# Optimization experiments

Measured on AMD Instinct MI355X. Metric: run time of the kernel, lower is better.

Reference implementation:

```python
import jax, jax.numpy as jnp
import numpy as np

# Module config (matches init_kwargs)
ANCHORS = np.array([[4.0, 4.0, 4.0], [8.0, 8.0, 8.0], [16.0, 16.0, 16.0]], dtype=np.float32)  # (w,h,d) per anchor
NUM_CLASSES = 1
IMG_SIZE = (96, 96, 96)  # (W, H, D)

B, A = 16, 3
ATTRS = 5 + NUM_CLASSES
D = H = W = 48


def setup_inputs() -> dict:
    key = jax.random.key(0)
    inp = jax.random.normal(key, (B, A * ATTRS, D, H, W), dtype=jnp.float32)
    return {"inp": inp}


def reference(inp):
    b, _, d, h, w = inp.shape
    stride_w = IMG_SIZE[0] / w
    stride_h = IMG_SIZE[1] / h
    stride_d = IMG_SIZE[2] / d

    # [B, A, D, H, W, attrs]
    pred = inp.reshape(b, A, ATTRS, d, h, w).transpose(0, 1, 3, 4, 5, 2)

    x = jax.nn.sigmoid(pred[..., 0])
    y = jax.nn.sigmoid(pred[..., 1])
    z = jax.nn.sigmoid(pred[..., 2])
    l = pred[..., 3]
    conf = jax.nn.sigmoid(pred[..., 4])
    pred_cls = jax.nn.sigmoid(pred[..., 5:])

    # Broadcast grids (replaces the nested python-loop fills)
    grid_x = jnp.arange(w, dtype=inp.dtype)                    # (W,) -> last axis
    grid_y = jnp.arange(h, dtype=inp.dtype)[:, None]           # (H,1)
    grid_z = jnp.arange(d, dtype=inp.dtype)[:, None, None]     # (D,1,1)

    # Original uses scaled anchor WIDTH for the length channel
    anchor_len = (jnp.asarray(ANCHORS[:, 0], dtype=inp.dtype) / stride_w)[None, :, None, None, None]

    bx = (x + grid_x) * stride_w
    by = (y + grid_y) * stride_h
    bz = (z + grid_z) * stride_d
    bl = jnp.exp(l) * anchor_len * stride_w

    boxes = jnp.stack([bx, by, bz, bl], axis=-1)  # [B,A,D,H,W,4]

    out = jnp.concatenate(
        [boxes.reshape(b, -1, 4), conf.reshape(b, -1, 1), pred_cls.reshape(b, -1, NUM_CLASSES)],
        axis=-1,
    )
    return out
```

## Files before the change

### kernel.cpp

```cpp
#include <hip/hip_runtime.h>


#define DHW   110592
#define HW48  2304
#define PAIRS 55296
#define NTOT  2654208

__device__ __forceinline__ float sigm(float v) {
    return 1.0f / (1.0f + __expf(-v));
}

__global__ __launch_bounds__(256) void DecodeBox_kernel(
    const float* __restrict__ in, float* __restrict__ out) {
    int t = blockIdx.x * blockDim.x + threadIdx.x;
    if (t >= NTOT) return;

    int s2 = t % PAIRS;
    int ba = t / PAIRS;
    int a  = ba % 3;
    int b  = ba / 3;

    int s  = 2 * s2;
    int x0 = s % 48;
    int y0 = (s / 48) % 48;
    int z0 = s / HW48;

    const float anchw = (a == 0) ? 4.0f : (a == 1) ? 8.0f : 16.0f;

    const float* ip = in + (size_t)(b * 18 + a * 6) * DHW + s;
    float2 tx = *(const float2*)(ip + 0 * DHW);
    float2 ty = *(const float2*)(ip + 1 * DHW);
    float2 tz = *(const float2*)(ip + 2 * DHW);
    float2 tl = *(const float2*)(ip + 3 * DHW);
    float2 tc = *(const float2*)(ip + 4 * DHW);
    float2 tk = *(const float2*)(ip + 5 * DHW);

    float bx0 = (sigm(tx.x) + (float)x0) * 2.0f;
    float by0 = (sigm(ty.x) + (float)y0) * 2.0f;
    float bz0 = (sigm(tz.x) + (float)z0) * 2.0f;
    float bl0 = __expf(tl.x) * anchw;
    float cf0 = sigm(tc.x);
    float cl0 = sigm(tk.x);
    float bx1 = (sigm(tx.y) + (float)(x0 + 1)) * 2.0f;
    float by1 = (sigm(ty.y) + (float)y0) * 2.0f;
    float bz1 = (sigm(tz.y) + (float)z0) * 2.0f;
    float bl1 = __expf(tl.y) * anchw;
    float cf1 = sigm(tc.y);
    float cl1 = sigm(tk.y);

    float4* op = (float4*)(out + (size_t)ba * (DHW * 6) + (size_t)12 * s2);
    op[0] = make_float4(bx0, by0, bz0, bl0);
    op[1] = make_float4(cf0, cl0, bx1, by1);
    op[2] = make_float4(bz1, bl1, cf1, cl1);
}

extern "C" void kernel_launch(void* const* d_in, const int* in_sizes, int n_in,
                              void* d_out, int out_size, void* d_ws, size_t ws_size,
                              hipStream_t stream) {
    const float* in = (const float*)d_in[0];
    float* out = (float*)d_out;
    const int threads = 256;
    const int blocks = (NTOT + threads - 1) / threads;
    DecodeBox_kernel<<<blocks, threads, 0, stream>>>(in, out);
}
```

Before: 223.1 us.

## Stage interleaved outputs through swizzled LDS for coalesced float4 stores

Each thread now processes four consecutive spatial positions with float4 loads instead of two with float2 loads. Outputs are written to shared memory with an XOR swizzle to avoid bank conflicts, then written back so consecutive lanes store consecutive float4s. This is meant to remove the strided 48-byte-per-lane store pattern that wastes write bandwidth. The cost is an LDS round-trip and a block barrier per tile.

```diff
diff --git a/kernel.cpp b/kernel.cpp
--- a/kernel.cpp
+++ b/kernel.cpp
@@ -3,55 +3,78 @@
 
 #define DHW   110592
 #define HW48  2304
-#define PAIRS 55296
-#define NTOT  2654208
+#define SPB   1024
+#define BPP   108
+#define F4B   1536
+#define F4P   165888
+#define NBLK  5184
 
 __device__ __forceinline__ float sigm(float v) {
     return 1.0f / (1.0f + __expf(-v));
 }
 
+__device__ __forceinline__ int swz(int i) {
+    return (i & ~7) | ((i ^ (i >> 3)) & 7);
+}
+
 __global__ __launch_bounds__(256) void DecodeBox_kernel(
     const float* __restrict__ in, float* __restrict__ out) {
-    int t = blockIdx.x * blockDim.x + threadIdx.x;
-    if (t >= NTOT) return;
+    __shared__ float4 lds[F4B];
 
-    int s2 = t % PAIRS;
-    int ba = t / PAIRS;
-    int a  = ba % 3;
-    int b  = ba / 3;
+    const int tid   = threadIdx.x;
+    const int blk   = blockIdx.x;
+    const int p     = blk / BPP;
+    const int chunk = blk - p * BPP;
+    const int a     = p % 3;
 
-    int s  = 2 * s2;
-    int x0 = s % 48;
-    int y0 = (s / 48) % 48;
-    int z0 = s / HW48;
-
+    const int S  = chunk * SPB + tid * 4;
+    const int x0 = S % 48;
+    const float yf = (float)((S / 48) % 48);
+    const float zf = (float)(S / HW48);
     const float anchw = (a == 0) ? 4.0f : (a == 1) ? 8.0f : 16.0f;
 
-    const float* ip = in + (size_t)(b * 18 + a * 6) * DHW + s;
-    float2 tx = *(const float2*)(ip + 0 * DHW);
-    float2 ty = *(const float2*)(ip + 1 * DHW);
-    float2 tz = *(const float2*)(ip + 2 * DHW);
-    float2 tl = *(const float2*)(ip + 3 * DHW);
-    float2 tc = *(const float2*)(ip + 4 * DHW);
-    float2 tk = *(const float2*)(ip + 5 * DHW);
+    const float* ip = in + (size_t)p * (6 * DHW) + S;
+    float4 tx = *(const float4*)(ip + 0 * DHW);
+    float4 ty = *(const float4*)(ip + 1 * DHW);
+    float4 tz = *(const float4*)(ip + 2 * DHW);
+    float4 tl = *(const float4*)(ip + 3 * DHW);
+    float4 tc = *(const float4*)(ip + 4 * DHW);
+    float4 tk = *(const float4*)(ip + 5 * DHW);
 
-    float bx0 = (sigm(tx.x) + (float)x0) * 2.0f;
-    float by0 = (sigm(ty.x) + (float)y0) * 2.0f;
-    float bz0 = (sigm(tz.x) + (float)z0) * 2.0f;
-    float bl0 = __expf(tl.x) * anchw;
-    float cf0 = sigm(tc.x);
-    float cl0 = sigm(tk.x);
-    float bx1 = (sigm(tx.y) + (float)(x0 + 1)) * 2.0f;
-    float by1 = (sigm(ty.y) + (float)y0) * 2.0f;
-    float bz1 = (sigm(tz.y) + (float)z0) * 2.0f;
-    float bl1 = __expf(tl.y) * anchw;
-    float cf1 = sigm(tc.y);
-    float cl1 = sigm(tk.y);
+    const float* txp = (const float*)&tx;
+    const float* typ = (const float*)&ty;
+    const float* tzp = (const float*)&tz;
+    const float* tlp = (const float*)&tl;
+    const float* tcp = (const float*)&tc;
+    const float* tkp = (const float*)&tk;
 
-    float4* op = (float4*)(out + (size_t)ba * (DHW * 6) + (size_t)12 * s2);
-    op[0] = make_float4(bx0, by0, bz0, bl0);
-    op[1] = make_float4(cf0, cl0, bx1, by1);
-    op[2] = make_float4(bz1, bl1, cf1, cl1);
+    float bx[4], by[4], bz[4], bl[4], cf[4], cl[4];
+#pragma unroll
+    for (int q = 0; q < 4; ++q) {
+        bx[q] = (sigm(txp[q]) + (float)(x0 + q)) * 2.0f;
+        by[q] = (sigm(typ[q]) + yf) * 2.0f;
+        bz[q] = (sigm(tzp[q]) + zf) * 2.0f;
+        bl[q] = __expf(tlp[q]) * anchw;
+        cf[q] = sigm(tcp[q]);
+        cl[q] = sigm(tkp[q]);
+    }
+
+    const int wb = 6 * tid;
+    lds[swz(wb + 0)] = make_float4(bx[0], by[0], bz[0], bl[0]);
+    lds[swz(wb + 1)] = make_float4(cf[0], cl[0], bx[1], by[1]);
+    lds[swz(wb + 2)] = make_float4(bz[1], bl[1], cf[1], cl[1]);
+    lds[swz(wb + 3)] = make_float4(bx[2], by[2], bz[2], bl[2]);
+    lds[swz(wb + 4)] = make_float4(cf[2], cl[2], bx[3], by[3]);
+    lds[swz(wb + 5)] = make_float4(bz[3], bl[3], cf[3], cl[3]);
+
+    __syncthreads();
+
+    float4* op = (float4*)out + (size_t)p * F4P + (size_t)chunk * F4B;
+#pragma unroll
+    for (int k = 0; k < 6; ++k) {
+        const int i = tid + 256 * k;
+        op[i] = lds[swz(i)];
+    }
 }
 
 extern "C" void kernel_launch(void* const* d_in, const int* in_sizes, int n_in,
@@ -59,7 +82,5 @@
                               hipStream_t stream) {
     const float* in = (const float*)d_in[0];
     float* out = (float*)d_out;
-    const int threads = 256;
-    const int blocks = (NTOT + threads - 1) / threads;
-    DecodeBox_kernel<<<blocks, threads, 0, stream>>>(in, out);
+    DecodeBox_kernel<<<NBLK, 256, 0, stream>>>(in, out);
 }
```

Result: no change. 220.3 us (-1.3%).
